# Optimization experiments

Hardware: AMD Instinct MI355X
Metric: run time of the kernel (lower is better)

The kernel has to match this reference:

```python
import jax, jax.numpy as jnp
import numpy as np

DISTANCE_SCALE = 25.0
VIEW_PE = 6
STEP = 0.02  # nominal ray-march step size used to scale dists


def positional_encoding(positions, freqs):
    # matches torch: (positions[..., None] * 2**k).reshape(..., freqs*C) -> [sin, cos]
    freq_bands = 2.0 ** jnp.arange(freqs, dtype=positions.dtype)
    pts = (positions[..., None] * freq_bands).reshape(positions.shape[:-1] + (freqs * positions.shape[-1],))
    return jnp.concatenate([jnp.sin(pts), jnp.cos(pts)], axis=-1)


def setup_inputs() -> dict:
    key = jax.random.key(0)
    ks = jax.random.split(key, 10)
    n_rays, n_samples, C, featureC = 4096, 256, 27, 128
    in_mlpC = 3 + 2 * VIEW_PE * 3 + C  # 66
    density_features = jax.random.normal(ks[0], (n_rays, n_samples), jnp.float32)
    app_features = jax.random.normal(ks[1], (n_rays, n_samples, C), jnp.float32)
    viewdirs = jax.random.normal(ks[2], (n_rays, 3), jnp.float32)
    viewdirs = viewdirs / jnp.linalg.norm(viewdirs, axis=-1, keepdims=True)
    dists = jax.random.uniform(ks[3], (n_rays, n_samples), jnp.float32) * STEP
    s1 = 1.0 / np.sqrt(in_mlpC)
    s2 = 1.0 / np.sqrt(featureC)
    W1 = jax.random.uniform(ks[4], (in_mlpC, featureC), jnp.float32, -s1, s1)
    b1 = jax.random.uniform(ks[5], (featureC,), jnp.float32, -s1, s1)
    W2 = jax.random.uniform(ks[6], (featureC, featureC), jnp.float32, -s2, s2)
    b2 = jax.random.uniform(ks[7], (featureC,), jnp.float32, -s2, s2)
    W3 = jax.random.uniform(ks[8], (featureC, 3), jnp.float32, -s2, s2)
    b3 = jnp.zeros((3,), jnp.float32)  # torch init: constant_(bias, 0)
    return {"density_features": density_features, "app_features": app_features,
            "viewdirs": viewdirs, "dists": dists,
            "W1": W1, "b1": b1, "W2": W2, "b2": b2, "W3": W3, "b3": b3}


def reference(density_features, app_features, viewdirs, dists, W1, b1, W2, b2, W3, b3):
    # feature2density (relu activation)
    sigma = jax.nn.relu(density_features)  # [R, S]
    # raw2alpha
    alpha = 1.0 - jnp.exp(-sigma * dists * DISTANCE_SCALE)  # [R, S]
    T = jnp.cumprod(jnp.concatenate([jnp.ones((alpha.shape[0], 1), alpha.dtype),
                                     1.0 - alpha + 1e-10], axis=-1), axis=-1)
    weights = alpha * T[:, :-1]  # [R, S]
    # radiance MLP over all sample points
    R, S, C = app_features.shape
    vd = jnp.broadcast_to(viewdirs[:, None, :], (R, S, 3))
    mlp_in = jnp.concatenate([app_features, vd, positional_encoding(vd, VIEW_PE)], axis=-1)  # [R,S,66]
    h = jax.nn.relu(mlp_in @ W1 + b1)
    h = jax.nn.relu(h @ W2 + b2)
    rgb = jax.nn.sigmoid(h @ W3 + b3)  # [R, S, 3]
    # composite (white background)
    acc_map = jnp.sum(weights, axis=-1)  # [R]
    rgb_map = jnp.einsum('rs,rsc->rc', weights, rgb)  # [R, 3]
    rgb_map = jnp.clip(rgb_map + (1.0 - acc_map[:, None]), 0.0, 1.0)
    return rgb_map
```

## Files before the change

### kernel.cpp

```cpp
#include <hip/hip_runtime.h>
#include <hip/hip_bf16.h>

typedef float f32x4 __attribute__((ext_vector_type(4)));
typedef short s16x8 __attribute__((ext_vector_type(8)));
typedef unsigned int u32;
typedef u32 u32x2 __attribute__((ext_vector_type(2)));

#define DIST_SCALE 25.0f

__device__ __forceinline__ unsigned short f2b(float f) {
  union { float f; unsigned u; } v; v.f = f;
  unsigned r = v.u + 0x7fffu + ((v.u >> 16) & 1u);
  return (unsigned short)(r >> 16);
}

__device__ __forceinline__ u32 cvtpk(float lo, float hi) {
  u32 r;
  asm("v_cvt_pk_bf16_f32 %0, %1, %2" : "=v"(r) : "v"(lo), "v"(hi));
  return r;
}

__device__ __forceinline__ int swzH(int s, int chbyte) {
  return (s * 256 + chbyte) ^ ((s & 7) << 4);
}

__global__ void prep_weights(const float* __restrict__ W1, const float* __restrict__ W2,
                             const float* __restrict__ W3, unsigned short* __restrict__ ws) {
  int t = blockIdx.x * 256 + threadIdx.x;
  int stride = gridDim.x * 256;
  for (int i = t; i < 128 * 32; i += stride) {
    int n = i >> 5, k = i & 31;
    ws[i] = (k < 27) ? f2b(W1[k * 128 + n]) : (unsigned short)0;
  }
  unsigned short* w2t = ws + 4096;
  for (int i = t; i < 128 * 128; i += stride) {
    int n = i >> 7, k = i & 127;
    w2t[i] = f2b(W2[k * 128 + n]);
  }
  unsigned short* w3p = ws + 4096 + 16384;
  for (int i = t; i < 4 * 16 * 32; i += stride) {
    int wv = i >> 9, rem = i & 511, n = rem >> 5, ks = rem & 31;
    int kg = ks >> 3, j = ks & 7;
    int ch = wv * 32 + ((j >> 2) << 4) + kg * 4 + (j & 3);
    w3p[i] = (n < 3) ? f2b(W3[ch * 3 + n]) : (unsigned short)0;
  }
}

__global__ void __launch_bounds__(256, 3) nerf_main(
    const float* __restrict__ dens, const float* __restrict__ app,
    const float* __restrict__ vdirs, const float* __restrict__ dists,
    const float* __restrict__ W1, const float* __restrict__ b1,
    const float* __restrict__ b2v, const float* __restrict__ b3v,
    const unsigned short* __restrict__ wsb, float* __restrict__ out) {
  __shared__ unsigned short Xs[64 * 40];
  __shared__ unsigned short HA[64 * 128];
  __shared__ float part[2][4 * 4 * 16 * 4];
  __shared__ float wbuf[256];
  __shared__ float hcbuf[128];
  __shared__ float featbuf[40];
  __shared__ float red[4][4];

  const int t = threadIdx.x;
  const int lane = t & 63;
  const int wv = t >> 6;
  const int r = blockIdx.x;

  const unsigned short* W1aT = wsb;
  const unsigned short* W2T = wsb + 4096;
  const unsigned short* W3P = wsb + 4096 + 16384;
  char* HAb = (char*)HA;

  const int cl = lane & 15;
  const int kg = lane >> 4;
  const int chBase = wv * 32;

  for (int i = t; i < 1280; i += 256) ((u32*)Xs)[i] = 0u;
  if (t < 39) {
    float val;
    if (t < 3) val = vdirs[r * 3 + t];
    else {
      int jj = t - 3;
      int trig = jj / 18;
      int rem = jj % 18;
      int c = rem / 6, k = rem % 6;
      float v = vdirs[r * 3 + c] * (float)(1 << k);
      val = trig ? cosf(v) : sinf(v);
    }
    featbuf[t] = val;
  }
  if (wv == 0) {
    const float4 dv = *(const float4*)(dens + (size_t)r * 256 + lane * 4);
    const float4 tv = *(const float4*)(dists + (size_t)r * 256 + lane * 4);
    float f[4], al[4];
    float dl[4] = {dv.x, dv.y, dv.z, dv.w};
    float tl[4] = {tv.x, tv.y, tv.z, tv.w};
    float p = 1.0f;
#pragma unroll
    for (int q = 0; q < 4; ++q) {
      float sg = fmaxf(dl[q], 0.0f);
      float e = __expf(-sg * tl[q] * DIST_SCALE);
      al[q] = 1.0f - e;
      f[q] = e + 1e-10f;
      p *= f[q];
    }
    float P = p;
#pragma unroll
    for (int dlt = 1; dlt < 64; dlt <<= 1) {
      float v = __shfl_up(P, dlt, 64);
      if (lane >= dlt) P *= v;
    }
    float E = __shfl_up(P, 1, 64);
    if (lane == 0) E = 1.0f;
    float tr = E;
#pragma unroll
    for (int q = 0; q < 4; ++q) { wbuf[lane * 4 + q] = al[q] * tr; tr *= f[q]; }
  }
  __syncthreads();
  if (t < 128) {
    float s = b1[t];
    for (int j = 0; j < 39; ++j) s += featbuf[j] * W1[(27 + j) * 128 + t];
    hcbuf[t] = s;
  }

  s16x8 w1f[2], w2f[2][4], w3s;
#pragma unroll
  for (int nt = 0; nt < 2; ++nt)
    w1f[nt] = *(const s16x8*)(W1aT + (chBase + nt * 16 + cl) * 32 + kg * 8);
#pragma unroll
  for (int nt = 0; nt < 2; ++nt)
#pragma unroll
    for (int kk = 0; kk < 4; ++kk)
      w2f[nt][kk] = *(const s16x8*)(W2T + (chBase + nt * 16 + cl) * 128 + kk * 32 + kg * 8);
  w3s = *(const s16x8*)(W3P + wv * 512 + cl * 32 + kg * 8);

  __syncthreads();

  float pr = 0.0f, pg = 0.0f, pb = 0.0f, pw = 0.0f;
  const float b30 = b3v[0], b31 = b3v[1], b32 = b3v[2];
  const f32x4 hc0 = *(const f32x4*)(hcbuf + chBase + kg * 4);
  const f32x4 hc1 = *(const f32x4*)(hcbuf + chBase + 16 + kg * 4);
  const f32x4 bb0 = *(const f32x4*)(b2v + chBase + kg * 4);
  const f32x4 bb1 = *(const f32x4*)(b2v + chBase + 16 + kg * 4);

  const float* rayBase = app + (size_t)r * 256 * 27;
  f32x4 L0 = *(const f32x4*)(rayBase + 4 * t);
  f32x4 L1 = {};
  if (t < 176) L1 = *(const f32x4*)(rayBase + 4 * (t + 256));

  for (int chunk = 0; chunk < 4; ++chunk) {
    {
      int e0 = 4 * t;
#pragma unroll
      for (int u = 0; u < 4; ++u) {
        unsigned e = e0 + u;
        unsigned s = e / 27u, c = e - s * 27u;
        *(unsigned short*)((char*)Xs + s * 80 + 2 * c) = f2b(L0[u]);
      }
      if (t < 176) {
        int e1 = 4 * (t + 256);
#pragma unroll
        for (int u = 0; u < 4; ++u) {
          unsigned e = e1 + u;
          unsigned s = e / 27u, c = e - s * 27u;
          *(unsigned short*)((char*)Xs + s * 80 + 2 * c) = f2b(L1[u]);
        }
      }
    }
    __syncthreads();

    if (chunk > 0) {
      const float* pp = part[(chunk - 1) & 1];
      f32x4 pv = *(const f32x4*)(pp + ((kg * 4 + wv) * 16 + cl) * 4);
      float v0 = pv[0], v1 = pv[1], v2 = pv[2];
      v0 += __shfl_xor(v0, 16, 64); v0 += __shfl_xor(v0, 32, 64);
      v1 += __shfl_xor(v1, 16, 64); v1 += __shfl_xor(v1, 32, 64);
      v2 += __shfl_xor(v2, 16, 64); v2 += __shfl_xor(v2, 32, 64);
      if (kg == 0) {
        float w = wbuf[(chunk - 1) * 64 + wv * 16 + cl];
        pw += w;
        pr += w / (1.0f + __expf(-(v0 + b30)));
        pg += w / (1.0f + __expf(-(v1 + b31)));
        pb += w / (1.0f + __expf(-(v2 + b32)));
      }
    }

    if (chunk < 3) {
      const float* slab = rayBase + (size_t)(chunk + 1) * 1728;
      L0 = *(const f32x4*)(slab + 4 * t);
      if (t < 176) L1 = *(const f32x4*)(slab + 4 * (t + 256));
    }

#pragma unroll
    for (int st = 0; st < 4; ++st) {
      const int s = st * 16 + cl;
      s16x8 xb = *(const s16x8*)((char*)Xs + s * 80 + kg * 16);
      f32x4 a0 = hc0, a1 = hc1;
      a0 = __builtin_amdgcn_mfma_f32_16x16x32_bf16(w1f[0], xb, a0, 0, 0, 0);
      a1 = __builtin_amdgcn_mfma_f32_16x16x32_bf16(w1f[1], xb, a1, 0, 0, 0);
      u32x2 pk0 = {cvtpk(fmaxf(a0[0], 0.0f), fmaxf(a0[1], 0.0f)),
                   cvtpk(fmaxf(a0[2], 0.0f), fmaxf(a0[3], 0.0f))};
      u32x2 pk1 = {cvtpk(fmaxf(a1[0], 0.0f), fmaxf(a1[1], 0.0f)),
                   cvtpk(fmaxf(a1[2], 0.0f), fmaxf(a1[3], 0.0f))};
      *(u32x2*)(HAb + swzH(s, (chBase + kg * 4) * 2)) = pk0;
      *(u32x2*)(HAb + swzH(s, (chBase + 16 + kg * 4) * 2)) = pk1;
    }
    __syncthreads();

#pragma unroll
    for (int st = 0; st < 4; ++st) {
      const int s = st * 16 + cl;
      s16x8 hbf[4];
#pragma unroll
      for (int kk = 0; kk < 4; ++kk)
        hbf[kk] = *(const s16x8*)(HAb + swzH(s, (kk * 32 + kg * 8) * 2));
      f32x4 a0 = bb0, a1 = bb1;
#pragma unroll
      for (int kk = 0; kk < 4; ++kk) {
        a0 = __builtin_amdgcn_mfma_f32_16x16x32_bf16(w2f[0][kk], hbf[kk], a0, 0, 0, 0);
        a1 = __builtin_amdgcn_mfma_f32_16x16x32_bf16(w2f[1][kk], hbf[kk], a1, 0, 0, 0);
      }
      union { u32 u[4]; s16x8 v; } b3;
      b3.u[0] = cvtpk(fmaxf(a0[0], 0.0f), fmaxf(a0[1], 0.0f));
      b3.u[1] = cvtpk(fmaxf(a0[2], 0.0f), fmaxf(a0[3], 0.0f));
      b3.u[2] = cvtpk(fmaxf(a1[0], 0.0f), fmaxf(a1[1], 0.0f));
      b3.u[3] = cvtpk(fmaxf(a1[2], 0.0f), fmaxf(a1[3], 0.0f));
      f32x4 p3 = {};
      p3 = __builtin_amdgcn_mfma_f32_16x16x32_bf16(w3s, b3.v, p3, 0, 0, 0);
      if (kg == 0)
        *(f32x4*)(part[chunk & 1] + ((wv * 4 + st) * 16 + cl) * 4) = p3;
    }
  }

  __syncthreads();
  {
    const float* pp = part[3 & 1];
    f32x4 pv = *(const f32x4*)(pp + ((kg * 4 + wv) * 16 + cl) * 4);
    float v0 = pv[0], v1 = pv[1], v2 = pv[2];
    v0 += __shfl_xor(v0, 16, 64); v0 += __shfl_xor(v0, 32, 64);
    v1 += __shfl_xor(v1, 16, 64); v1 += __shfl_xor(v1, 32, 64);
    v2 += __shfl_xor(v2, 16, 64); v2 += __shfl_xor(v2, 32, 64);
    if (kg == 0) {
      float w = wbuf[3 * 64 + wv * 16 + cl];
      pw += w;
      pr += w / (1.0f + __expf(-(v0 + b30)));
      pg += w / (1.0f + __expf(-(v1 + b31)));
      pb += w / (1.0f + __expf(-(v2 + b32)));
    }
  }

  if (kg == 0) {
#pragma unroll
    for (int d = 1; d < 16; d <<= 1) {
      pr += __shfl_xor(pr, d, 64);
      pg += __shfl_xor(pg, d, 64);
      pb += __shfl_xor(pb, d, 64);
      pw += __shfl_xor(pw, d, 64);
    }
    if (lane == 0) { red[wv][0] = pr; red[wv][1] = pg; red[wv][2] = pb; red[wv][3] = pw; }
  }
  __syncthreads();
  if (t == 0) {
    float R = 0, G = 0, B = 0, W = 0;
#pragma unroll
    for (int w = 0; w < 4; ++w) { R += red[w][0]; G += red[w][1]; B += red[w][2]; W += red[w][3]; }
    float bg = 1.0f - W;
    out[r * 3 + 0] = fminf(fmaxf(R + bg, 0.0f), 1.0f);
    out[r * 3 + 1] = fminf(fmaxf(G + bg, 0.0f), 1.0f);
    out[r * 3 + 2] = fminf(fmaxf(B + bg, 0.0f), 1.0f);
  }
}

extern "C" void kernel_launch(void* const* d_in, const int* in_sizes, int n_in,
                              void* d_out, int out_size, void* d_ws, size_t ws_size,
                              hipStream_t stream) {
  const float* dens = (const float*)d_in[0];
  const float* app  = (const float*)d_in[1];
  const float* vd   = (const float*)d_in[2];
  const float* dist = (const float*)d_in[3];
  const float* W1   = (const float*)d_in[4];
  const float* b1   = (const float*)d_in[5];
  const float* W2   = (const float*)d_in[6];
  const float* b2   = (const float*)d_in[7];
  const float* W3   = (const float*)d_in[8];
  const float* b3   = (const float*)d_in[9];
  unsigned short* wsb = (unsigned short*)d_ws;

  prep_weights<<<32, 256, 0, stream>>>(W1, W2, W3, wsb);
  nerf_main<<<4096, 256, 0, stream>>>(dens, app, vd, dist, W1, b1, b2, b3, wsb, (float*)d_out);
}
```

Measured before the change: 81.31 us.

## Reduce layer-3 partials each chunk with single buffer and simplify Xs indexing

Swaps the double-buffered partial-sum scratch, which was consumed one chunk late, for a single packed 3-float-per-sample buffer that is reduced right after each chunk behind an extra barrier. This shrinks shared memory and removes the deferred epilogue. The f32-to-bf16 staging also now does one divide by 27 per thread and derives the other three addresses with a wrap adjustment instead of four divides. The cost is one more __syncthreads per chunk, which removes the overlap of the reduction with the next chunk's work.

```diff
diff --git a/kernel.cpp b/kernel.cpp
--- a/kernel.cpp
+++ b/kernel.cpp
@@ -54,7 +54,7 @@
     const unsigned short* __restrict__ wsb, float* __restrict__ out) {
   __shared__ unsigned short Xs[64 * 40];
   __shared__ unsigned short HA[64 * 128];
-  __shared__ float part[2][4 * 4 * 16 * 4];
+  __shared__ float part[4 * 64 * 3];
   __shared__ float wbuf[256];
   __shared__ float hcbuf[128];
   __shared__ float featbuf[40];
@@ -148,41 +148,28 @@
   if (t < 176) L1 = *(const f32x4*)(rayBase + 4 * (t + 256));
 
   for (int chunk = 0; chunk < 4; ++chunk) {
+    const int sBase = chunk * 64;
     {
-      int e0 = 4 * t;
-#pragma unroll
-      for (int u = 0; u < 4; ++u) {
-        unsigned e = e0 + u;
-        unsigned s = e / 27u, c = e - s * 27u;
-        *(unsigned short*)((char*)Xs + s * 80 + 2 * c) = f2b(L0[u]);
+      unsigned e0 = 4u * (unsigned)t;
+      unsigned s0 = e0 / 27u, c0 = e0 - s0 * 27u;
+      unsigned base = s0 * 80u + 2u * c0;
+#pragma unroll
+      for (int u2 = 0; u2 < 4; ++u2) {
+        unsigned a = base + 2u * u2 + ((c0 + u2 >= 27u) ? 26u : 0u);
+        *(unsigned short*)((char*)Xs + a) = f2b(L0[u2]);
       }
       if (t < 176) {
-        int e1 = 4 * (t + 256);
-#pragma unroll
-        for (int u = 0; u < 4; ++u) {
-          unsigned e = e1 + u;
-          unsigned s = e / 27u, c = e - s * 27u;
-          *(unsigned short*)((char*)Xs + s * 80 + 2 * c) = f2b(L1[u]);
+        unsigned e1 = 4u * (unsigned)(t + 256);
+        unsigned s1 = e1 / 27u, c1 = e1 - s1 * 27u;
+        unsigned bs1 = s1 * 80u + 2u * c1;
+#pragma unroll
+        for (int u2 = 0; u2 < 4; ++u2) {
+          unsigned a = bs1 + 2u * u2 + ((c1 + u2 >= 27u) ? 26u : 0u);
+          *(unsigned short*)((char*)Xs + a) = f2b(L1[u2]);
         }
       }
     }
     __syncthreads();
-
-    if (chunk > 0) {
-      const float* pp = part[(chunk - 1) & 1];
-      f32x4 pv = *(const f32x4*)(pp + ((kg * 4 + wv) * 16 + cl) * 4);
-      float v0 = pv[0], v1 = pv[1], v2 = pv[2];
-      v0 += __shfl_xor(v0, 16, 64); v0 += __shfl_xor(v0, 32, 64);
-      v1 += __shfl_xor(v1, 16, 64); v1 += __shfl_xor(v1, 32, 64);
-      v2 += __shfl_xor(v2, 16, 64); v2 += __shfl_xor(v2, 32, 64);
-      if (kg == 0) {
-        float w = wbuf[(chunk - 1) * 64 + wv * 16 + cl];
-        pw += w;
-        pr += w / (1.0f + __expf(-(v0 + b30)));
-        pg += w / (1.0f + __expf(-(v1 + b31)));
-        pb += w / (1.0f + __expf(-(v2 + b32)));
-      }
-    }
 
     if (chunk < 3) {
       const float* slab = rayBase + (size_t)(chunk + 1) * 1728;
@@ -226,25 +213,26 @@
       b3.u[3] = cvtpk(fmaxf(a1[2], 0.0f), fmaxf(a1[3], 0.0f));
       f32x4 p3 = {};
       p3 = __builtin_amdgcn_mfma_f32_16x16x32_bf16(w3s, b3.v, p3, 0, 0, 0);
-      if (kg == 0)
-        *(f32x4*)(part[chunk & 1] + ((wv * 4 + st) * 16 + cl) * 4) = p3;
-    }
-  }
-
-  __syncthreads();
-  {
-    const float* pp = part[3 & 1];
-    f32x4 pv = *(const f32x4*)(pp + ((kg * 4 + wv) * 16 + cl) * 4);
-    float v0 = pv[0], v1 = pv[1], v2 = pv[2];
-    v0 += __shfl_xor(v0, 16, 64); v0 += __shfl_xor(v0, 32, 64);
-    v1 += __shfl_xor(v1, 16, 64); v1 += __shfl_xor(v1, 32, 64);
-    v2 += __shfl_xor(v2, 16, 64); v2 += __shfl_xor(v2, 32, 64);
-    if (kg == 0) {
-      float w = wbuf[3 * 64 + wv * 16 + cl];
-      pw += w;
-      pr += w / (1.0f + __expf(-(v0 + b30)));
-      pg += w / (1.0f + __expf(-(v1 + b31)));
-      pb += w / (1.0f + __expf(-(v2 + b32)));
+      if (kg == 0) {
+        float* pp = part + (wv * 64 + s) * 3;
+        pp[0] = p3[0]; pp[1] = p3[1]; pp[2] = p3[2];
+      }
+    }
+    __syncthreads();
+
+    {
+      const float* pp = part + ((kg * 64) + wv * 16 + cl) * 3;
+      float v0 = pp[0], v1 = pp[1], v2 = pp[2];
+      v0 += __shfl_xor(v0, 16, 64); v0 += __shfl_xor(v0, 32, 64);
+      v1 += __shfl_xor(v1, 16, 64); v1 += __shfl_xor(v1, 32, 64);
+      v2 += __shfl_xor(v2, 16, 64); v2 += __shfl_xor(v2, 32, 64);
+      if (kg == 0) {
+        float w = wbuf[sBase + wv * 16 + cl];
+        pw += w;
+        pr += w / (1.0f + __expf(-(v0 + b30)));
+        pg += w / (1.0f + __expf(-(v1 + b31)));
+        pb += w / (1.0f + __expf(-(v2 + b32)));
+      }
     }
   }
 
```

Result: no change. 81.67 us (+0.4%).
